# Optimization experiments

Measured on AMD Instinct MI355X. Metric: run time of the kernel, lower is better.

Reference implementation:

```python
import jax, jax.numpy as jnp
import numpy as np

B, N, S, D = 8, 325, 64, 256
H = 8
HD = D // H  # head_dim = 32


def setup_inputs() -> dict:
    key = jax.random.key(0)
    ks = jax.random.split(key, 5)
    x = jax.random.normal(ks[0], (B, N, S, D), dtype=jnp.float32)
    # nn.Linear params: weight [out, in], bias [out]
    w_qkv = jax.random.normal(ks[1], (3 * D, D), dtype=jnp.float32) * (1.0 / np.sqrt(D))
    b_qkv = jax.random.normal(ks[2], (3 * D,), dtype=jnp.float32) * 0.01
    w_proj = jax.random.normal(ks[3], (D, D), dtype=jnp.float32) * (1.0 / np.sqrt(D))
    b_proj = jax.random.normal(ks[4], (D,), dtype=jnp.float32) * 0.01
    return {"x": x, "w_qkv": w_qkv, "b_qkv": b_qkv, "w_proj": w_proj, "b_proj": b_proj}


def reference(x, w_qkv, b_qkv, w_proj, b_proj):
    b, n, s, d = x.shape
    scale = (d // H) ** -0.5
    xf = x.reshape(b * n, s, d)                              # [BN, S, D]
    qkv = jnp.einsum('bsd,ed->bse', xf, w_qkv) + b_qkv       # [BN, S, 3D]
    qkv = qkv.reshape(b * n, s, 3, H, HD)
    qkv = jnp.transpose(qkv, (2, 0, 3, 1, 4))                # [3, BN, H, S, HD]
    q, k, v = qkv[0], qkv[1], qkv[2]
    attn = jnp.einsum('bhqe,bhke->bhqk', q, k) * scale       # [BN, H, S, S]
    attn = jax.nn.softmax(attn, axis=-1)
    out = jnp.einsum('bhqk,bhke->bhqe', attn, v)             # [BN, H, S, HD]
    out = jnp.transpose(out, (0, 2, 1, 3)).reshape(b * n, s, d)
    out = jnp.einsum('bsd,ed->bse', out, w_proj) + b_proj
    return out.reshape(b, n, s, d)
```

## Files before the change

kernel.cpp:

```cpp
#include <hip/hip_runtime.h>
#include <hip/hip_bf16.h>


namespace {

constexpr int S_LEN = 64;
constexpr int DM    = 256;
constexpr int SD    = S_LEN * DM;
constexpr int NQKV  = 3 * DM * DM;

typedef float f32x4 __attribute__((ext_vector_type(4)));
typedef short s16x8 __attribute__((ext_vector_type(8)));

union BF2 { __hip_bfloat162 h; unsigned u; };
__device__ __forceinline__ unsigned pkbf2(float a, float b) {
  float2 t; t.x = a; t.y = b;
  BF2 cv; cv.h = __float22bfloat162_rn(t);
  return cv.u;
}

__device__ __forceinline__ void bar_lgkm() {
  asm volatile("s_waitcnt lgkmcnt(0)" ::: "memory");
  __builtin_amdgcn_sched_barrier(0);
  __builtin_amdgcn_s_barrier();
  __builtin_amdgcn_sched_barrier(0);
}

__device__ __forceinline__ s16x8 xpose_frag(f32x4 a0, f32x4 a1, int c, int g) {
  const int src0 = ((g & 1) << 5) + c;
  const int src1 = src0 + 16;
  unsigned p00 = pkbf2(a0[0], a0[1]);
  unsigned p01 = pkbf2(a0[2], a0[3]);
  unsigned p10 = pkbf2(a1[0], a1[1]);
  unsigned p11 = pkbf2(a1[2], a1[3]);
  const bool hi = (g & 2) != 0;
  unsigned w0a = (unsigned)__shfl((int)p00, src0);
  unsigned w0b = (unsigned)__shfl((int)p10, src0);
  unsigned w1a = (unsigned)__shfl((int)p01, src0);
  unsigned w1b = (unsigned)__shfl((int)p11, src0);
  unsigned w2a = (unsigned)__shfl((int)p00, src1);
  unsigned w2b = (unsigned)__shfl((int)p10, src1);
  unsigned w3a = (unsigned)__shfl((int)p01, src1);
  unsigned w3b = (unsigned)__shfl((int)p11, src1);
  union { s16x8 v; unsigned u[4]; } r;
  r.u[0] = hi ? w0b : w0a;
  r.u[1] = hi ? w1b : w1a;
  r.u[2] = hi ? w2b : w2a;
  r.u[3] = hi ? w3b : w3a;
  return r.v;
}

__device__ __forceinline__ int wswz(int row, int u) {
  return row * 32 + ((u ^ ((row >> 1) & 3)) << 3);
}

}

__global__ void ta_prep_weights(const float* __restrict__ wqkv,
                                const float* __restrict__ wproj,
                                unsigned short* __restrict__ wsb) {
  const int i = (blockIdx.x * 256 + (int)threadIdx.x) * 4;
  f32x4 v = (i < NQKV) ? *(const f32x4*)(wqkv + i)
                       : *(const f32x4*)(wproj + (i - NQKV));
  unsigned u0 = pkbf2(v[0], v[1]);
  unsigned u1 = pkbf2(v[2], v[3]);
  *(uint2*)(wsb + i) = make_uint2(u0, u1);
}

__global__ void __launch_bounds__(512, 1)
ta_fused_kernel(const float* __restrict__ x,
                const unsigned short* __restrict__ wq_bf,
                const float* __restrict__ bqkv,
                const unsigned short* __restrict__ wp_bf,
                const float* __restrict__ bproj,
                float* __restrict__ out)
{
  __shared__ __align__(16) unsigned short lds[65536];

  const int bn = blockIdx.x;
  const int tid = (int)threadIdx.x;
  const int w = tid >> 6;
  const int l = tid & 63;
  const int g = l >> 4;
  const int c = l & 15;
  const int c7s = (c & 7) << 3;
  const int h = w;

  unsigned short* __restrict__ xls = lds;
  unsigned short* wbuf[2] = { lds + 16384, lds + 40960 };

  const float* __restrict__ xb = x + (size_t)bn * SD;

  s16x8 wst[6];
#pragma unroll
  for (int i = 0; i < 6; ++i) {
    const int idx = i * 512 + tid, row = idx >> 2, gl = idx & 3;
    wst[i] = *(const s16x8*)&wq_bf[row * 256 + 0 * 32 + gl * 8];
  }

#pragma unroll
  for (int it = 0; it < 4; ++it) {
    const int e = (it * 512 + tid) * 8;
    const int row = e >> 8;
    f32x4 a = *(const f32x4*)(xb + e);
    f32x4 b = *(const f32x4*)(xb + e + 4);
    union { s16x8 v; unsigned u[4]; } r;
    r.u[0] = pkbf2(a[0], a[1]); r.u[1] = pkbf2(a[2], a[3]);
    r.u[2] = pkbf2(b[0], b[1]); r.u[3] = pkbf2(b[2], b[3]);
    *(s16x8*)&xls[e ^ ((row & 7) << 3)] = r.v;
  }
  bar_lgkm();

#pragma unroll
  for (int i = 0; i < 6; ++i) {
    const int idx = i * 512 + tid, row = idx >> 2, gl = idx & 3;
    *(s16x8*)&wbuf[0][wswz(row, gl)] = wst[i];
  }
#pragma unroll
  for (int i = 0; i < 6; ++i) {
    const int idx = i * 512 + tid, row = idx >> 2, gl = idx & 3;
    wst[i] = *(const s16x8*)&wq_bf[row * 256 + 1 * 32 + gl * 8];
  }
  bar_lgkm();

  f32x4 aq[2][4], ak[2][4], av[4][2];
#pragma unroll
  for (int t = 0; t < 2; ++t)
#pragma unroll
    for (int nj = 0; nj < 4; ++nj) {
      aq[t][nj] = f32x4{0.f, 0.f, 0.f, 0.f};
      ak[t][nj] = f32x4{0.f, 0.f, 0.f, 0.f};
    }
#pragma unroll
  for (int mt = 0; mt < 4; ++mt)
#pragma unroll
    for (int t = 0; t < 2; ++t) av[mt][t] = f32x4{0.f, 0.f, 0.f, 0.f};

#pragma unroll
  for (int ks = 0; ks < 8; ++ks) {
    const unsigned short* wb = wbuf[ks & 1];
    const int kof = ks * 32 + g * 8;
    s16x8 bx[4];
#pragma unroll
    for (int nj = 0; nj < 4; ++nj) {
      const int row = 16 * nj + c;
      bx[nj] = *(const s16x8*)&xls[(row * 256 + kof) ^ c7s];
    }
#pragma unroll
    for (int t = 0; t < 2; ++t) {
      s16x8 awq = *(const s16x8*)&wb[wswz((2 * h + t) * 16 + c, g)];
      s16x8 awk = *(const s16x8*)&wb[wswz(256 + 32 * h + 16 * t + c, g)];
      s16x8 awv = *(const s16x8*)&wb[wswz(512 + 32 * h + 16 * t + c, g)];
#pragma unroll
      for (int nj = 0; nj < 4; ++nj) {
        aq[t][nj] = __builtin_amdgcn_mfma_f32_16x16x32_bf16(awq, bx[nj], aq[t][nj], 0, 0, 0);
        ak[t][nj] = __builtin_amdgcn_mfma_f32_16x16x32_bf16(awk, bx[nj], ak[t][nj], 0, 0, 0);
        av[nj][t] = __builtin_amdgcn_mfma_f32_16x16x32_bf16(bx[nj], awv, av[nj][t], 0, 0, 0);
      }
    }
    if (ks < 7) {
#pragma unroll
      for (int i = 0; i < 6; ++i) {
        const int idx = i * 512 + tid, row = idx >> 2, gl = idx & 3;
        *(s16x8*)&wbuf[(ks + 1) & 1][wswz(row, gl)] = wst[i];
      }
    }
    if (ks < 6) {
#pragma unroll
      for (int i = 0; i < 6; ++i) {
        const int idx = i * 512 + tid, row = idx >> 2, gl = idx & 3;
        wst[i] = *(const s16x8*)&wq_bf[row * 256 + (ks + 2) * 32 + gl * 8];
      }
    }
    bar_lgkm();
  }

  s16x8 pst[2];
#pragma unroll
  for (int i = 0; i < 2; ++i) {
    const int idx = i * 512 + tid, row = idx >> 2, gl = idx & 3;
    pst[i] = *(const s16x8*)&wp_bf[row * 256 + 0 * 32 + gl * 8];
  }

#pragma unroll
  for (int t = 0; t < 2; ++t) {
    f32x4 bq = *(const f32x4*)(bqkv + (2 * h + t) * 16 + 4 * g);
    f32x4 bk = *(const f32x4*)(bqkv + 256 + 32 * h + 16 * t + 4 * g);
#pragma unroll
    for (int nj = 0; nj < 4; ++nj) {
      aq[t][nj] += bq;
      ak[t][nj] += bk;
    }
  }
  {
    const float bv0 = bqkv[512 + 32 * h + c];
    const float bv1 = bqkv[512 + 32 * h + 16 + c];
#pragma unroll
    for (int mt = 0; mt < 4; ++mt)
#pragma unroll
      for (int r = 0; r < 4; ++r) {
        av[mt][0][r] += bv0;
        av[mt][1][r] += bv1;
      }
  }

  s16x8 qa[4], ka[4];
#pragma unroll
  for (int i = 0; i < 4; ++i) {
    qa[i] = xpose_frag(aq[0][i], aq[1][i], c, g);
    ka[i] = xpose_frag(ak[0][i], ak[1][i], c, g);
  }

  f32x4 sa[4][4];
#pragma unroll
  for (int ki = 0; ki < 4; ++ki)
#pragma unroll
    for (int qi = 0; qi < 4; ++qi) {
      f32x4 z = f32x4{0.f, 0.f, 0.f, 0.f};
      sa[ki][qi] = __builtin_amdgcn_mfma_f32_16x16x32_bf16(ka[ki], qa[qi], z, 0, 0, 0);
    }

  const float sc = 0.17677669529663687f * 1.4426950408889634f;
  float inv[4];
#pragma unroll
  for (int qi = 0; qi < 4; ++qi) {
    float m = sa[0][qi][0];
#pragma unroll
    for (int ki = 0; ki < 4; ++ki)
#pragma unroll
      for (int r = 0; r < 4; ++r) m = fmaxf(m, sa[ki][qi][r]);
    m = fmaxf(m, __shfl_xor(m, 16));
    m = fmaxf(m, __shfl_xor(m, 32));
    float s = 0.0f;
#pragma unroll
    for (int ki = 0; ki < 4; ++ki)
#pragma unroll
      for (int r = 0; r < 4; ++r) {
        float pv = exp2f((sa[ki][qi][r] - m) * sc);
        sa[ki][qi][r] = pv;
        s += pv;
      }
    s += __shfl_xor(s, 16);
    s += __shfl_xor(s, 32);
    inv[qi] = 1.0f / s;
  }

  s16x8 pa[4][2];
#pragma unroll
  for (int mi = 0; mi < 4; ++mi) {
    const float iv = inv[mi];
#pragma unroll
    for (int ks2 = 0; ks2 < 2; ++ks2) {
      f32x4 v0 = sa[2 * ks2][mi] * iv;
      f32x4 v1 = sa[2 * ks2 + 1][mi] * iv;
      pa[mi][ks2] = xpose_frag(v0, v1, c, g);
    }
  }

  s16x8 vb[2][2];
#pragma unroll
  for (int nd = 0; nd < 2; ++nd)
#pragma unroll
    for (int ks2 = 0; ks2 < 2; ++ks2)
      vb[nd][ks2] = xpose_frag(av[2 * ks2][nd], av[2 * ks2 + 1][nd], c, g);

  f32x4 oa[4][2];
#pragma unroll
  for (int mi = 0; mi < 4; ++mi)
#pragma unroll
    for (int nd = 0; nd < 2; ++nd) oa[mi][nd] = f32x4{0.f, 0.f, 0.f, 0.f};
#pragma unroll
  for (int ks2 = 0; ks2 < 2; ++ks2)
#pragma unroll
    for (int mi = 0; mi < 4; ++mi)
#pragma unroll
      for (int nd = 0; nd < 2; ++nd)
        oa[mi][nd] = __builtin_amdgcn_mfma_f32_16x16x32_bf16(pa[mi][ks2], vb[nd][ks2], oa[mi][nd], 0, 0, 0);

  unsigned obp[4][2][2];
#pragma unroll
  for (int mi = 0; mi < 4; ++mi)
#pragma unroll
    for (int nd = 0; nd < 2; ++nd) {
      obp[mi][nd][0] = pkbf2(oa[mi][nd][0], oa[mi][nd][1]);
      obp[mi][nd][1] = pkbf2(oa[mi][nd][2], oa[mi][nd][3]);
    }

#pragma unroll
  for (int mi = 0; mi < 4; ++mi)
#pragma unroll
    for (int nd = 0; nd < 2; ++nd)
#pragma unroll
      for (int r = 0; r < 4; ++r) {
        const int q = 16 * mi + 4 * g + r;
        const int feat = h * 32 + 16 * nd + c;
        unsigned val = obp[mi][nd][r >> 1] >> (16 * (r & 1));
        xls[(q * 256 + feat) ^ ((q & 7) << 3)] = (unsigned short)val;
      }
#pragma unroll
  for (int i = 0; i < 2; ++i) {
    const int idx = i * 512 + tid, row = idx >> 2, gl = idx & 3;
    *(s16x8*)&wbuf[0][wswz(row, gl)] = pst[i];
  }
#pragma unroll
  for (int i = 0; i < 2; ++i) {
    const int idx = i * 512 + tid, row = idx >> 2, gl = idx & 3;
    pst[i] = *(const s16x8*)&wp_bf[row * 256 + 1 * 32 + gl * 8];
  }
  bar_lgkm();

  f32x4 pacc[2][4];
#pragma unroll
  for (int ti = 0; ti < 2; ++ti)
#pragma unroll
    for (int nj = 0; nj < 4; ++nj) pacc[ti][nj] = f32x4{0.f, 0.f, 0.f, 0.f};

#pragma unroll
  for (int ks = 0; ks < 8; ++ks) {
    const unsigned short* wb = wbuf[ks & 1];
    const int kof = ks * 32 + 8 * g;
    s16x8 bx[4];
#pragma unroll
    for (int nj = 0; nj < 4; ++nj) {
      const int row = 16 * nj + c;
      bx[nj] = *(const s16x8*)&xls[(row * 256 + kof) ^ c7s];
    }
#pragma unroll
    for (int ti = 0; ti < 2; ++ti) {
      s16x8 aw = *(const s16x8*)&wb[wswz((2 * w + ti) * 16 + c, g)];
#pragma unroll
      for (int nj = 0; nj < 4; ++nj)
        pacc[ti][nj] = __builtin_amdgcn_mfma_f32_16x16x32_bf16(aw, bx[nj], pacc[ti][nj], 0, 0, 0);
    }
    if (ks < 7) {
#pragma unroll
      for (int i = 0; i < 2; ++i) {
        const int idx = i * 512 + tid, row = idx >> 2, gl = idx & 3;
        *(s16x8*)&wbuf[(ks + 1) & 1][wswz(row, gl)] = pst[i];
      }
    }
    if (ks < 6) {
#pragma unroll
      for (int i = 0; i < 2; ++i) {
        const int idx = i * 512 + tid, row = idx >> 2, gl = idx & 3;
        pst[i] = *(const s16x8*)&wp_bf[row * 256 + (ks + 2) * 32 + gl * 8];
      }
    }
    bar_lgkm();
  }

  float* ldsf = (float*)wbuf[0];
  float* __restrict__ ob = out + (size_t)bn * SD;
#pragma unroll
  for (int H = 0; H < 2; ++H) {
#pragma unroll
    for (int ti = 0; ti < 2; ++ti) {
      const int e0 = (2 * w + ti) * 16 + 4 * g;
      f32x4 bp = *(const f32x4*)(bproj + e0);
#pragma unroll
      for (int nj = 2 * H; nj < 2 * H + 2; ++nj) {
        const int lr = 16 * (nj - 2 * H) + c;
        f32x4 v;
        v[0] = pacc[ti][nj][0] + bp[0];
        v[1] = pacc[ti][nj][1] + bp[1];
        v[2] = pacc[ti][nj][2] + bp[2];
        v[3] = pacc[ti][nj][3] + bp[3];
        *(f32x4*)&ldsf[(lr * 256 + e0) ^ ((lr & 7) << 2)] = v;
      }
    }
    bar_lgkm();
#pragma unroll
    for (int it = 0; it < 4; ++it) {
      const int i = (it * 512 + tid) * 4;
      const int lr = i >> 8;
      f32x4 v = *(const f32x4*)&ldsf[i ^ ((lr & 7) << 2)];
      *(f32x4*)(ob + H * 8192 + i) = v;
    }
    if (H == 0) bar_lgkm();
  }
}

extern "C" void kernel_launch(void* const* d_in, const int* in_sizes, int n_in,
                              void* d_out, int out_size, void* d_ws, size_t ws_size,
                              hipStream_t stream) {
  (void)n_in; (void)ws_size; (void)out_size;
  const float* x     = (const float*)d_in[0];
  const float* wqkv  = (const float*)d_in[1];
  const float* bqkv  = (const float*)d_in[2];
  const float* wproj = (const float*)d_in[3];
  const float* bproj = (const float*)d_in[4];
  float* out = (float*)d_out;

  unsigned short* wsb = (unsigned short*)d_ws;
  const unsigned short* wq_bf = wsb;
  const unsigned short* wp_bf = wsb + NQKV;

  hipLaunchKernelGGL(ta_prep_weights, dim3(256), dim3(256), 0, stream, wqkv, wproj, wsb);

  const int bn_total = in_sizes[0] / SD;
  hipLaunchKernelGGL(ta_fused_kernel, dim3(bn_total), dim3(512), 0, stream,
                     x, wq_bf, bqkv, wp_bf, bproj, out);
}
```

Measured before the change: 242.2 us.

## Process two sequences per block and stream pre-swizzled weights via direct-to-LDS loads

Each workgroup now handles two (b,n) sequences, so every bf16 weight slice staged in LDS feeds twice as many MFMAs, halving weight traffic per sequence. The prep kernel now writes weights in a k-slice-major, pre-swizzled tile order, so the fused kernel can copy them straight into LDS with global_load_lds instead of routing them through registers. A single weight buffer replaces the double buffer, with extra barriers placed around each refill. The cost is higher register pressure from doubled accumulators, and the grid shrinks to about 1300 blocks; it also assumes an even bn count.

```diff
diff --git a/kernel.cpp b/kernel.cpp
--- a/kernel.cpp
+++ b/kernel.cpp
@@ -7,7 +7,7 @@
 constexpr int S_LEN = 64;
 constexpr int DM    = 256;
 constexpr int SD    = S_LEN * DM;
-constexpr int NQKV  = 3 * DM * DM;
+constexpr int QKV_UNITS = 8 * 768 * 4;
 
 typedef float f32x4 __attribute__((ext_vector_type(4)));
 typedef short s16x8 __attribute__((ext_vector_type(8)));
@@ -54,30 +54,116 @@
   return row * 32 + ((u ^ ((row >> 1) & 3)) << 3);
 }
 
+__device__ __forceinline__ void attn_middle(
+    const f32x4 (&aq)[2][4], const f32x4 (&ak)[2][4], const s16x8 (&vb)[2][2],
+    int c, int g, unsigned (&obp)[4][2][2])
+{
+  s16x8 qa[4], ka[4];
+#pragma unroll
+  for (int i = 0; i < 4; ++i) {
+    qa[i] = xpose_frag(aq[0][i], aq[1][i], c, g);
+    ka[i] = xpose_frag(ak[0][i], ak[1][i], c, g);
+  }
+  f32x4 sa[4][4];
+#pragma unroll
+  for (int ki = 0; ki < 4; ++ki)
+#pragma unroll
+    for (int qi = 0; qi < 4; ++qi) {
+      f32x4 z = f32x4{0.f, 0.f, 0.f, 0.f};
+      sa[ki][qi] = __builtin_amdgcn_mfma_f32_16x16x32_bf16(ka[ki], qa[qi], z, 0, 0, 0);
+    }
+  const float sc = 0.17677669529663687f * 1.4426950408889634f;
+  float inv[4];
+#pragma unroll
+  for (int qi = 0; qi < 4; ++qi) {
+    float m = sa[0][qi][0];
+#pragma unroll
+    for (int ki = 0; ki < 4; ++ki)
+#pragma unroll
+      for (int r = 0; r < 4; ++r) m = fmaxf(m, sa[ki][qi][r]);
+    m = fmaxf(m, __shfl_xor(m, 16));
+    m = fmaxf(m, __shfl_xor(m, 32));
+    float s = 0.0f;
+#pragma unroll
+    for (int ki = 0; ki < 4; ++ki)
+#pragma unroll
+      for (int r = 0; r < 4; ++r) {
+        float pv = exp2f((sa[ki][qi][r] - m) * sc);
+        sa[ki][qi][r] = pv;
+        s += pv;
+      }
+    s += __shfl_xor(s, 16);
+    s += __shfl_xor(s, 32);
+    inv[qi] = 1.0f / s;
+  }
+  s16x8 pa[4][2];
+#pragma unroll
+  for (int mi = 0; mi < 4; ++mi) {
+    const float iv = inv[mi];
+#pragma unroll
+    for (int ks2 = 0; ks2 < 2; ++ks2) {
+      f32x4 v0 = sa[2 * ks2][mi] * iv;
+      f32x4 v1 = sa[2 * ks2 + 1][mi] * iv;
+      pa[mi][ks2] = xpose_frag(v0, v1, c, g);
+    }
+  }
+  f32x4 oa[4][2];
+#pragma unroll
+  for (int mi = 0; mi < 4; ++mi)
+#pragma unroll
+    for (int nd = 0; nd < 2; ++nd) oa[mi][nd] = f32x4{0.f, 0.f, 0.f, 0.f};
+#pragma unroll
+  for (int ks2 = 0; ks2 < 2; ++ks2)
+#pragma unroll
+    for (int mi = 0; mi < 4; ++mi)
+#pragma unroll
+      for (int nd = 0; nd < 2; ++nd)
+        oa[mi][nd] = __builtin_amdgcn_mfma_f32_16x16x32_bf16(pa[mi][ks2], vb[nd][ks2], oa[mi][nd], 0, 0, 0);
+#pragma unroll
+  for (int mi = 0; mi < 4; ++mi)
+#pragma unroll
+    for (int nd = 0; nd < 2; ++nd) {
+      obp[mi][nd][0] = pkbf2(oa[mi][nd][0], oa[mi][nd][1]);
+      obp[mi][nd][1] = pkbf2(oa[mi][nd][2], oa[mi][nd][3]);
+    }
+}
+
 }
 
 __global__ void ta_prep_weights(const float* __restrict__ wqkv,
                                 const float* __restrict__ wproj,
                                 unsigned short* __restrict__ wsb) {
-  const int i = (blockIdx.x * 256 + (int)threadIdx.x) * 4;
-  f32x4 v = (i < NQKV) ? *(const f32x4*)(wqkv + i)
-                       : *(const f32x4*)(wproj + (i - NQKV));
-  unsigned u0 = pkbf2(v[0], v[1]);
-  unsigned u1 = pkbf2(v[2], v[3]);
-  *(uint2*)(wsb + i) = make_uint2(u0, u1);
+  const int o = blockIdx.x * 256 + (int)threadIdx.x;
+  const float* src;
+  if (o < QKV_UNITS) {
+    const int ks = o / 3072, rem = o - ks * 3072;
+    const int row = rem >> 2, u = rem & 3;
+    const int s = (row >> 1) & 3;
+    src = wqkv + row * 256 + ks * 32 + ((u ^ s) << 3);
+  } else {
+    const int p = o - QKV_UNITS;
+    const int ks = p >> 10, rem = p & 1023;
+    const int row = rem >> 2, u = rem & 3;
+    const int s = (row >> 1) & 3;
+    src = wproj + row * 256 + ks * 32 + ((u ^ s) << 3);
+  }
+  f32x4 a = *(const f32x4*)src;
+  f32x4 b = *(const f32x4*)(src + 4);
+  *(uint4*)(wsb + (size_t)o * 8) =
+      make_uint4(pkbf2(a[0], a[1]), pkbf2(a[2], a[3]),
+                 pkbf2(b[0], b[1]), pkbf2(b[2], b[3]));
 }
 
 __global__ void __launch_bounds__(512, 1)
 ta_fused_kernel(const float* __restrict__ x,
-                const unsigned short* __restrict__ wq_bf,
+                const unsigned short* __restrict__ wqt,
                 const float* __restrict__ bqkv,
-                const unsigned short* __restrict__ wp_bf,
+                const unsigned short* __restrict__ wpt,
                 const float* __restrict__ bproj,
                 float* __restrict__ out)
 {
-  __shared__ __align__(16) unsigned short lds[65536];
-
-  const int bn = blockIdx.x;
+  __shared__ __align__(16) unsigned short lds[57344];
+
   const int tid = (int)threadIdx.x;
   const int w = tid >> 6;
   const int l = tid & 63;
@@ -86,295 +172,234 @@
   const int c7s = (c & 7) << 3;
   const int h = w;
 
-  unsigned short* __restrict__ xls = lds;
-  unsigned short* wbuf[2] = { lds + 16384, lds + 40960 };
-
-  const float* __restrict__ xb = x + (size_t)bn * SD;
-
-  s16x8 wst[6];
+  unsigned short* xls0 = lds;
+  unsigned short* xls1 = lds + 16384;
+  unsigned short* wb   = lds + 32768;
+
+  const int bn0 = blockIdx.x * 2;
+  const float* __restrict__ xbA = x + (size_t)bn0 * SD;
+  const float* __restrict__ xbB = xbA + SD;
+
 #pragma unroll
   for (int i = 0; i < 6; ++i) {
-    const int idx = i * 512 + tid, row = idx >> 2, gl = idx & 3;
-    wst[i] = *(const s16x8*)&wq_bf[row * 256 + 0 * 32 + gl * 8];
-  }
-
-#pragma unroll
-  for (int it = 0; it < 4; ++it) {
-    const int e = (it * 512 + tid) * 8;
-    const int row = e >> 8;
-    f32x4 a = *(const f32x4*)(xb + e);
-    f32x4 b = *(const f32x4*)(xb + e + 4);
-    union { s16x8 v; unsigned u[4]; } r;
-    r.u[0] = pkbf2(a[0], a[1]); r.u[1] = pkbf2(a[2], a[3]);
-    r.u[2] = pkbf2(b[0], b[1]); r.u[3] = pkbf2(b[2], b[3]);
-    *(s16x8*)&xls[e ^ ((row & 7) << 3)] = r.v;
-  }
-  bar_lgkm();
-
-#pragma unroll
-  for (int i = 0; i < 6; ++i) {
-    const int idx = i * 512 + tid, row = idx >> 2, gl = idx & 3;
-    *(s16x8*)&wbuf[0][wswz(row, gl)] = wst[i];
-  }
-#pragma unroll
-  for (int i = 0; i < 6; ++i) {
-    const int idx = i * 512 + tid, row = idx >> 2, gl = idx & 3;
-    wst[i] = *(const s16x8*)&wq_bf[row * 256 + 1 * 32 + gl * 8];
-  }
-  bar_lgkm();
-
-  f32x4 aq[2][4], ak[2][4], av[4][2];
-#pragma unroll
-  for (int t = 0; t < 2; ++t)
-#pragma unroll
-    for (int nj = 0; nj < 4; ++nj) {
-      aq[t][nj] = f32x4{0.f, 0.f, 0.f, 0.f};
-      ak[t][nj] = f32x4{0.f, 0.f, 0.f, 0.f};
-    }
-#pragma unroll
-  for (int mt = 0; mt < 4; ++mt)
-#pragma unroll
-    for (int t = 0; t < 2; ++t) av[mt][t] = f32x4{0.f, 0.f, 0.f, 0.f};
+    const int n = i * 512 + tid;
+    __builtin_amdgcn_global_load_lds(
+        (const __attribute__((address_space(1))) unsigned int*)(wqt + (size_t)(0 * 3072 + n) * 8),
+        (__attribute__((address_space(3))) unsigned int*)(wb + n * 8), 16, 0, 0);
+  }
+
+#pragma unroll
+  for (int s2 = 0; s2 < 2; ++s2) {
+    const float* __restrict__ xb = s2 ? xbB : xbA;
+    unsigned short* __restrict__ xd = s2 ? xls1 : xls0;
+#pragma unroll
+    for (int it = 0; it < 4; ++it) {
+      const int e = (it * 512 + tid) * 8;
+      const int row = e >> 8;
+      f32x4 a = *(const f32x4*)(xb + e);
+      f32x4 b = *(const f32x4*)(xb + e + 4);
+      union { s16x8 v; unsigned u[4]; } r;
+      r.u[0] = pkbf2(a[0], a[1]); r.u[1] = pkbf2(a[2], a[3]);
+      r.u[2] = pkbf2(b[0], b[1]); r.u[3] = pkbf2(b[2], b[3]);
+      *(s16x8*)&xd[e ^ ((row & 7) << 3)] = r.v;
+    }
+  }
+  __syncthreads();
+
+  f32x4 aq[2][2][4], ak[2][2][4], av[2][4][2];
+#pragma unroll
+  for (int s2 = 0; s2 < 2; ++s2) {
+#pragma unroll
+    for (int t = 0; t < 2; ++t)
+#pragma unroll
+      for (int nj = 0; nj < 4; ++nj) {
+        aq[s2][t][nj] = f32x4{0.f, 0.f, 0.f, 0.f};
+        ak[s2][t][nj] = f32x4{0.f, 0.f, 0.f, 0.f};
+      }
+#pragma unroll
+    for (int mt = 0; mt < 4; ++mt)
+#pragma unroll
+      for (int t = 0; t < 2; ++t) av[s2][mt][t] = f32x4{0.f, 0.f, 0.f, 0.f};
+  }
 
 #pragma unroll
   for (int ks = 0; ks < 8; ++ks) {
-    const unsigned short* wb = wbuf[ks & 1];
+    s16x8 awq[2], awk[2], awv[2];
+#pragma unroll
+    for (int t = 0; t < 2; ++t) {
+      awq[t] = *(const s16x8*)&wb[wswz((2 * h + t) * 16 + c, g)];
+      awk[t] = *(const s16x8*)&wb[wswz(256 + 32 * h + 16 * t + c, g)];
+      awv[t] = *(const s16x8*)&wb[wswz(512 + 32 * h + 16 * t + c, g)];
+    }
+    bar_lgkm();
+    if (ks < 7) {
+#pragma unroll
+      for (int i = 0; i < 6; ++i) {
+        const int n = i * 512 + tid;
+        __builtin_amdgcn_global_load_lds(
+            (const __attribute__((address_space(1))) unsigned int*)(wqt + (size_t)((ks + 1) * 3072 + n) * 8),
+            (__attribute__((address_space(3))) unsigned int*)(wb + n * 8), 16, 0, 0);
+      }
+    }
     const int kof = ks * 32 + g * 8;
-    s16x8 bx[4];
-#pragma unroll
-    for (int nj = 0; nj < 4; ++nj) {
-      const int row = 16 * nj + c;
-      bx[nj] = *(const s16x8*)&xls[(row * 256 + kof) ^ c7s];
-    }
+#pragma unroll
+    for (int s2 = 0; s2 < 2; ++s2) {
+      const unsigned short* xd = s2 ? xls1 : xls0;
+      s16x8 bx[4];
+#pragma unroll
+      for (int nj = 0; nj < 4; ++nj) {
+        const int row = 16 * nj + c;
+        bx[nj] = *(const s16x8*)&xd[(row * 256 + kof) ^ c7s];
+      }
+#pragma unroll
+      for (int t = 0; t < 2; ++t)
+#pragma unroll
+        for (int nj = 0; nj < 4; ++nj) {
+          aq[s2][t][nj] = __builtin_amdgcn_mfma_f32_16x16x32_bf16(awq[t], bx[nj], aq[s2][t][nj], 0, 0, 0);
+          ak[s2][t][nj] = __builtin_amdgcn_mfma_f32_16x16x32_bf16(awk[t], bx[nj], ak[s2][t][nj], 0, 0, 0);
+          av[s2][nj][t] = __builtin_amdgcn_mfma_f32_16x16x32_bf16(bx[nj], awv[t], av[s2][nj][t], 0, 0, 0);
+        }
+    }
+    __syncthreads();
+  }
+
+#pragma unroll
+  for (int i = 0; i < 2; ++i) {
+    const int n = i * 512 + tid;
+    __builtin_amdgcn_global_load_lds(
+        (const __attribute__((address_space(1))) unsigned int*)(wpt + (size_t)(0 * 1024 + n) * 8),
+        (__attribute__((address_space(3))) unsigned int*)(wb + n * 8), 16, 0, 0);
+  }
+
+#pragma unroll
+  for (int s2 = 0; s2 < 2; ++s2) {
 #pragma unroll
     for (int t = 0; t < 2; ++t) {
-      s16x8 awq = *(const s16x8*)&wb[wswz((2 * h + t) * 16 + c, g)];
-      s16x8 awk = *(const s16x8*)&wb[wswz(256 + 32 * h + 16 * t + c, g)];
-      s16x8 awv = *(const s16x8*)&wb[wswz(512 + 32 * h + 16 * t + c, g)];
+      f32x4 bq = *(const f32x4*)(bqkv + (2 * h + t) * 16 + 4 * g);
+      f32x4 bk = *(const f32x4*)(bqkv + 256 + 32 * h + 16 * t + 4 * g);
 #pragma unroll
       for (int nj = 0; nj < 4; ++nj) {
-        aq[t][nj] = __builtin_amdgcn_mfma_f32_16x16x32_bf16(awq, bx[nj], aq[t][nj], 0, 0, 0);
-        ak[t][nj] = __builtin_amdgcn_mfma_f32_16x16x32_bf16(awk, bx[nj], ak[t][nj], 0, 0, 0);
-        av[nj][t] = __builtin_amdgcn_mfma_f32_16x16x32_bf16(bx[nj], awv, av[nj][t], 0, 0, 0);
-      }
-    }
-    if (ks < 7) {
-#pragma unroll
-      for (int i = 0; i < 6; ++i) {
-        const int idx = i * 512 + tid, row = idx >> 2, gl = idx & 3;
-        *(s16x8*)&wbuf[(ks + 1) & 1][wswz(row, gl)] = wst[i];
-      }
-    }
-    if (ks < 6) {
-#pragma unroll
-      for (int i = 0; i < 6; ++i) {
-        const int idx = i * 512 + tid, row = idx >> 2, gl = idx & 3;
-        wst[i] = *(const s16x8*)&wq_bf[row * 256 + (ks + 2) * 32 + gl * 8];
-      }
-    }
-    bar_lgkm();
-  }
-
-  s16x8 pst[2];
-#pragma unroll
-  for (int i = 0; i < 2; ++i) {
-    const int idx = i * 512 + tid, row = idx >> 2, gl = idx & 3;
-    pst[i] = *(const s16x8*)&wp_bf[row * 256 + 0 * 32 + gl * 8];
-  }
-
-#pragma unroll
-  for (int t = 0; t < 2; ++t) {
-    f32x4 bq = *(const f32x4*)(bqkv + (2 * h + t) * 16 + 4 * g);
-    f32x4 bk = *(const f32x4*)(bqkv + 256 + 32 * h + 16 * t + 4 * g);
-#pragma unroll
-    for (int nj = 0; nj < 4; ++nj) {
-      aq[t][nj] += bq;
-      ak[t][nj] += bk;
-    }
-  }
-  {
+        aq[s2][t][nj] += bq;
+        ak[s2][t][nj] += bk;
+      }
+    }
     const float bv0 = bqkv[512 + 32 * h + c];
     const float bv1 = bqkv[512 + 32 * h + 16 + c];
 #pragma unroll
     for (int mt = 0; mt < 4; ++mt)
 #pragma unroll
       for (int r = 0; r < 4; ++r) {
-        av[mt][0][r] += bv0;
-        av[mt][1][r] += bv1;
-      }
-  }
-
-  s16x8 qa[4], ka[4];
-#pragma unroll
-  for (int i = 0; i < 4; ++i) {
-    qa[i] = xpose_frag(aq[0][i], aq[1][i], c, g);
-    ka[i] = xpose_frag(ak[0][i], ak[1][i], c, g);
-  }
-
-  f32x4 sa[4][4];
-#pragma unroll
-  for (int ki = 0; ki < 4; ++ki)
-#pragma unroll
-    for (int qi = 0; qi < 4; ++qi) {
-      f32x4 z = f32x4{0.f, 0.f, 0.f, 0.f};
-      sa[ki][qi] = __builtin_amdgcn_mfma_f32_16x16x32_bf16(ka[ki], qa[qi], z, 0, 0, 0);
-    }
-
-  const float sc = 0.17677669529663687f * 1.4426950408889634f;
-  float inv[4];
-#pragma unroll
-  for (int qi = 0; qi < 4; ++qi) {
-    float m = sa[0][qi][0];
-#pragma unroll
-    for (int ki = 0; ki < 4; ++ki)
-#pragma unroll
-      for (int r = 0; r < 4; ++r) m = fmaxf(m, sa[ki][qi][r]);
-    m = fmaxf(m, __shfl_xor(m, 16));
-    m = fmaxf(m, __shfl_xor(m, 32));
-    float s = 0.0f;
-#pragma unroll
-    for (int ki = 0; ki < 4; ++ki)
-#pragma unroll
-      for (int r = 0; r < 4; ++r) {
-        float pv = exp2f((sa[ki][qi][r] - m) * sc);
-        sa[ki][qi][r] = pv;
-        s += pv;
-      }
-    s += __shfl_xor(s, 16);
-    s += __shfl_xor(s, 32);
-    inv[qi] = 1.0f / s;
-  }
-
-  s16x8 pa[4][2];
-#pragma unroll
-  for (int mi = 0; mi < 4; ++mi) {
-    const float iv = inv[mi];
-#pragma unroll
-    for (int ks2 = 0; ks2 < 2; ++ks2) {
-      f32x4 v0 = sa[2 * ks2][mi] * iv;
-      f32x4 v1 = sa[2 * ks2 + 1][mi] * iv;
-      pa[mi][ks2] = xpose_frag(v0, v1, c, g);
-    }
-  }
-
-  s16x8 vb[2][2];
-#pragma unroll
-  for (int nd = 0; nd < 2; ++nd)
-#pragma unroll
-    for (int ks2 = 0; ks2 < 2; ++ks2)
-      vb[nd][ks2] = xpose_frag(av[2 * ks2][nd], av[2 * ks2 + 1][nd], c, g);
-
-  f32x4 oa[4][2];
-#pragma unroll
-  for (int mi = 0; mi < 4; ++mi)
-#pragma unroll
-    for (int nd = 0; nd < 2; ++nd) oa[mi][nd] = f32x4{0.f, 0.f, 0.f, 0.f};
-#pragma unroll
-  for (int ks2 = 0; ks2 < 2; ++ks2)
+        av[s2][mt][0][r] += bv0;
+        av[s2][mt][1][r] += bv1;
+      }
+  }
+
+  s16x8 vb[2][2][2];
+#pragma unroll
+  for (int s2 = 0; s2 < 2; ++s2)
+#pragma unroll
+    for (int nd = 0; nd < 2; ++nd)
+#pragma unroll
+      for (int ks2 = 0; ks2 < 2; ++ks2)
+        vb[s2][nd][ks2] = xpose_frag(av[s2][2 * ks2][nd], av[s2][2 * ks2 + 1][nd], c, g);
+
+  unsigned obp[2][4][2][2];
+  attn_middle(aq[0], ak[0], vb[0], c, g, obp[0]);
+  attn_middle(aq[1], ak[1], vb[1], c, g, obp[1]);
+
+#pragma unroll
+  for (int s2 = 0; s2 < 2; ++s2) {
+    unsigned short* att = s2 ? xls1 : xls0;
 #pragma unroll
     for (int mi = 0; mi < 4; ++mi)
 #pragma unroll
       for (int nd = 0; nd < 2; ++nd)
-        oa[mi][nd] = __builtin_amdgcn_mfma_f32_16x16x32_bf16(pa[mi][ks2], vb[nd][ks2], oa[mi][nd], 0, 0, 0);
-
-  unsigned obp[4][2][2];
-#pragma unroll
-  for (int mi = 0; mi < 4; ++mi)
-#pragma unroll
-    for (int nd = 0; nd < 2; ++nd) {
-      obp[mi][nd][0] = pkbf2(oa[mi][nd][0], oa[mi][nd][1]);
-      obp[mi][nd][1] = pkbf2(oa[mi][nd][2], oa[mi][nd][3]);
-    }
-
-#pragma unroll
-  for (int mi = 0; mi < 4; ++mi)
-#pragma unroll
-    for (int nd = 0; nd < 2; ++nd)
-#pragma unroll
-      for (int r = 0; r < 4; ++r) {
-        const int q = 16 * mi + 4 * g + r;
-        const int feat = h * 32 + 16 * nd + c;
-        unsigned val = obp[mi][nd][r >> 1] >> (16 * (r & 1));
-        xls[(q * 256 + feat) ^ ((q & 7) << 3)] = (unsigned short)val;
-      }
-#pragma unroll
-  for (int i = 0; i < 2; ++i) {
-    const int idx = i * 512 + tid, row = idx >> 2, gl = idx & 3;
-    *(s16x8*)&wbuf[0][wswz(row, gl)] = pst[i];
-  }
-#pragma unroll
-  for (int i = 0; i < 2; ++i) {
-    const int idx = i * 512 + tid, row = idx >> 2, gl = idx & 3;
-    pst[i] = *(const s16x8*)&wp_bf[row * 256 + 1 * 32 + gl * 8];
-  }
-  bar_lgkm();
-
-  f32x4 pacc[2][4];
-#pragma unroll
-  for (int ti = 0; ti < 2; ++ti)
-#pragma unroll
-    for (int nj = 0; nj < 4; ++nj) pacc[ti][nj] = f32x4{0.f, 0.f, 0.f, 0.f};
+#pragma unroll
+        for (int r = 0; r < 4; ++r) {
+          const int q = 16 * mi + 4 * g + r;
+          const int feat = h * 32 + 16 * nd + c;
+          unsigned val = obp[s2][mi][nd][r >> 1] >> (16 * (r & 1));
+          att[(q * 256 + feat) ^ ((q & 7) << 3)] = (unsigned short)val;
+        }
+  }
+  __syncthreads();
+
+  f32x4 pacc[2][2][4];
+#pragma unroll
+  for (int s2 = 0; s2 < 2; ++s2)
+#pragma unroll
+    for (int ti = 0; ti < 2; ++ti)
+#pragma unroll
+      for (int nj = 0; nj < 4; ++nj) pacc[s2][ti][nj] = f32x4{0.f, 0.f, 0.f, 0.f};
 
 #pragma unroll
   for (int ks = 0; ks < 8; ++ks) {
-    const unsigned short* wb = wbuf[ks & 1];
+    s16x8 aw[2];
+#pragma unroll
+    for (int ti = 0; ti < 2; ++ti)
+      aw[ti] = *(const s16x8*)&wb[wswz((2 * w + ti) * 16 + c, g)];
+    bar_lgkm();
+    if (ks < 7) {
+#pragma unroll
+      for (int i = 0; i < 2; ++i) {
+        const int n = i * 512 + tid;
+        __builtin_amdgcn_global_load_lds(
+            (const __attribute__((address_space(1))) unsigned int*)(wpt + (size_t)((ks + 1) * 1024 + n) * 8),
+            (__attribute__((address_space(3))) unsigned int*)(wb + n * 8), 16, 0, 0);
+      }
+    }
     const int kof = ks * 32 + 8 * g;
-    s16x8 bx[4];
-#pragma unroll
-    for (int nj = 0; nj < 4; ++nj) {
-      const int row = 16 * nj + c;
-      bx[nj] = *(const s16x8*)&xls[(row * 256 + kof) ^ c7s];
-    }
-#pragma unroll
-    for (int ti = 0; ti < 2; ++ti) {
-      s16x8 aw = *(const s16x8*)&wb[wswz((2 * w + ti) * 16 + c, g)];
-#pragma unroll
-      for (int nj = 0; nj < 4; ++nj)
-        pacc[ti][nj] = __builtin_amdgcn_mfma_f32_16x16x32_bf16(aw, bx[nj], pacc[ti][nj], 0, 0, 0);
-    }
-    if (ks < 7) {
-#pragma unroll
-      for (int i = 0; i < 2; ++i) {
-        const int idx = i * 512 + tid, row = idx >> 2, gl = idx & 3;
-        *(s16x8*)&wbuf[(ks + 1) & 1][wswz(row, gl)] = pst[i];
-      }
-    }
-    if (ks < 6) {
-#pragma unroll
-      for (int i = 0; i < 2; ++i) {
-        const int idx = i * 512 + tid, row = idx >> 2, gl = idx & 3;
-        pst[i] = *(const s16x8*)&wp_bf[row * 256 + (ks + 2) * 32 + gl * 8];
+#pragma unroll
+    for (int s2 = 0; s2 < 2; ++s2) {
+      const unsigned short* att = s2 ? xls1 : xls0;
+      s16x8 bx[4];
+#pragma unroll
+      for (int nj = 0; nj < 4; ++nj) {
+        const int row = 16 * nj + c;
+        bx[nj] = *(const s16x8*)&att[(row * 256 + kof) ^ c7s];
+      }
+#pragma unroll
+      for (int ti = 0; ti < 2; ++ti)
+#pragma unroll
+        for (int nj = 0; nj < 4; ++nj)
+          pacc[s2][ti][nj] = __builtin_amdgcn_mfma_f32_16x16x32_bf16(aw[ti], bx[nj], pacc[s2][ti][nj], 0, 0, 0);
+    }
+    __syncthreads();
+  }
+
+#pragma unroll
+  for (int H = 0; H < 2; ++H) {
+#pragma unroll
+    for (int s2 = 0; s2 < 2; ++s2) {
+      float* ldsf = (float*)(s2 ? xls1 : xls0);
+#pragma unroll
+      for (int ti = 0; ti < 2; ++ti) {
+        const int e0 = (2 * w + ti) * 16 + 4 * g;
+        f32x4 bp = *(const f32x4*)(bproj + e0);
+#pragma unroll
+        for (int nj = 2 * H; nj < 2 * H + 2; ++nj) {
+          const int lr = 16 * (nj - 2 * H) + c;
+          f32x4 v;
+          v[0] = pacc[s2][ti][nj][0] + bp[0];
+          v[1] = pacc[s2][ti][nj][1] + bp[1];
+          v[2] = pacc[s2][ti][nj][2] + bp[2];
+          v[3] = pacc[s2][ti][nj][3] + bp[3];
+          *(f32x4*)&ldsf[(lr * 256 + e0) ^ ((lr & 7) << 2)] = v;
+        }
       }
     }
     bar_lgkm();
-  }
-
-  float* ldsf = (float*)wbuf[0];
-  float* __restrict__ ob = out + (size_t)bn * SD;
-#pragma unroll
-  for (int H = 0; H < 2; ++H) {
-#pragma unroll
-    for (int ti = 0; ti < 2; ++ti) {
-      const int e0 = (2 * w + ti) * 16 + 4 * g;
-      f32x4 bp = *(const f32x4*)(bproj + e0);
-#pragma unroll
-      for (int nj = 2 * H; nj < 2 * H + 2; ++nj) {
-        const int lr = 16 * (nj - 2 * H) + c;
-        f32x4 v;
-        v[0] = pacc[ti][nj][0] + bp[0];
-        v[1] = pacc[ti][nj][1] + bp[1];
-        v[2] = pacc[ti][nj][2] + bp[2];
-        v[3] = pacc[ti][nj][3] + bp[3];
-        *(f32x4*)&ldsf[(lr * 256 + e0) ^ ((lr & 7) << 2)] = v;
-      }
-    }
-    bar_lgkm();
-#pragma unroll
-    for (int it = 0; it < 4; ++it) {
-      const int i = (it * 512 + tid) * 4;
-      const int lr = i >> 8;
-      f32x4 v = *(const f32x4*)&ldsf[i ^ ((lr & 7) << 2)];
-      *(f32x4*)(ob + H * 8192 + i) = v;
+#pragma unroll
+    for (int s2 = 0; s2 < 2; ++s2) {
+      const float* ldsf = (const float*)(s2 ? xls1 : xls0);
+      float* __restrict__ ob = out + (size_t)(bn0 + s2) * SD;
+#pragma unroll
+      for (int it = 0; it < 4; ++it) {
+        const int i = (it * 512 + tid) * 4;
+        const int lr = i >> 8;
+        f32x4 v = *(const f32x4*)&ldsf[i ^ ((lr & 7) << 2)];
+        *(f32x4*)(ob + H * 8192 + i) = v;
+      }
     }
     if (H == 0) bar_lgkm();
   }
@@ -392,12 +417,12 @@
   float* out = (float*)d_out;
 
   unsigned short* wsb = (unsigned short*)d_ws;
-  const unsigned short* wq_bf = wsb;
-  const unsigned short* wp_bf = wsb + NQKV;
-
-  hipLaunchKernelGGL(ta_prep_weights, dim3(256), dim3(256), 0, stream, wqkv, wproj, wsb);
+  const unsigned short* wqt = wsb;
+  const unsigned short* wpt = wsb + QKV_UNITS * 8;
+
+  hipLaunchKernelGGL(ta_prep_weights, dim3(128), dim3(256), 0, stream, wqkv, wproj, wsb);
 
   const int bn_total = in_sizes[0] / SD;
-  hipLaunchKernelGGL(ta_fused_kernel, dim3(bn_total), dim3(512), 0, stream,
-                     x, wq_bf, bqkv, wp_bf, bproj, out);
-}
+  hipLaunchKernelGGL(ta_fused_kernel, dim3(bn_total / 2), dim3(512), 0, stream,
+                     x, wqt, bqkv, wpt, bproj, out);
+}
```

Measured after the change: 375.0 us. +54.8%, slower.
